# Optimization experiments

Measured on AMD Instinct MI355X. Metric: run time of the kernel, lower is better.

The kernel has to match this reference:

```python
import jax, jax.numpy as jnp
import numpy as np

H = 1024
V = 50257
S = 2048


def setup_inputs() -> dict:
    key = jax.random.key(0)
    ks = jax.random.split(key, 20)
    sd = 1.0 / np.sqrt(H)
    inp = {
        "input": jax.random.randint(ks[0], (1,), 0, V, dtype=jnp.int64) if jax.config.jax_enable_x64 else jax.random.randint(ks[0], (1,), 0, V, dtype=jnp.int32),
        "hidden": jax.random.normal(ks[1], (1, 1, H), dtype=jnp.float32),
        "encoder_hiddens": jax.random.normal(ks[2], (S, H), dtype=jnp.float32),
        "emb": jax.random.normal(ks[3], (V, H), dtype=jnp.float32),
        "Ua_w": jax.random.normal(ks[4], (H, H), dtype=jnp.float32) * sd,
        "Ua_b": jax.random.normal(ks[5], (H,), dtype=jnp.float32) * sd,
        "Wa_w": jax.random.normal(ks[6], (H, H), dtype=jnp.float32) * sd,
        "Wa_b": jax.random.normal(ks[7], (H,), dtype=jnp.float32) * sd,
        "va": jax.random.normal(ks[8], (1, H), dtype=jnp.float32),
        "comb_w": jax.random.normal(ks[9], (H, 2 * H), dtype=jnp.float32) * sd,
        "comb_b": jax.random.normal(ks[10], (H,), dtype=jnp.float32) * sd,
        "gru_w_ih": jax.random.normal(ks[11], (3 * H, H), dtype=jnp.float32) * sd,
        "gru_w_hh": jax.random.normal(ks[12], (3 * H, H), dtype=jnp.float32) * sd,
        "gru_b_ih": jax.random.normal(ks[13], (3 * H,), dtype=jnp.float32) * sd,
        "gru_b_hh": jax.random.normal(ks[14], (3 * H,), dtype=jnp.float32) * sd,
        "out_w": jax.random.normal(ks[15], (V, 2 * H), dtype=jnp.float32) * sd,
        "out_b": jax.random.normal(ks[16], (V,), dtype=jnp.float32) * sd,
    }
    return inp


def reference(input, hidden, encoder_hiddens, emb, Ua_w, Ua_b, Wa_w, Wa_b, va,
              comb_w, comb_b, gru_w_ih, gru_w_hh, gru_b_ih, gru_b_hh, out_w, out_b):
    # embedded: [1,1,H]  (dropout is identity in eval / p handled at train time)
    embedded = emb[input].reshape(1, 1, H)
    enc = encoder_hiddens[:, None, :]  # [S,1,H]
    # Bahdanau scores: tanh(Ua(enc) + Wa(hidden)) -> [S,1,H]
    scores = jnp.tanh(enc @ Ua_w.T + Ua_b + hidden @ Wa_w.T + Wa_b)
    # torch.inner(va [1,H], scores [S,1,H]) -> [1,S,1]; softmax over S
    attn_weights = jax.nn.softmax(jnp.einsum('oh,sbh->osb', va, scores), axis=1)
    # context: sum_s attn[1,S,1] * enc[S,H] -> [1,H]
    context = jnp.sum(attn_weights * encoder_hiddens, axis=1)
    # combine + relu -> GRU input x: [1,H]
    x = jax.nn.relu(jnp.concatenate([embedded[0], context], axis=1) @ comb_w.T + comb_b)
    # single GRU cell step (PyTorch gate layout: r, z, n)
    h0 = hidden[0]  # [1,H]
    gi = x @ gru_w_ih.T + gru_b_ih
    gh = h0 @ gru_w_hh.T + gru_b_hh
    i_r, i_z, i_n = jnp.split(gi, 3, axis=1)
    h_r, h_z, h_n = jnp.split(gh, 3, axis=1)
    r = jax.nn.sigmoid(i_r + h_r)
    z = jax.nn.sigmoid(i_z + h_z)
    n = jnp.tanh(i_n + r * h_n)
    h_new = (1.0 - z) * n + z * h0  # [1,H]
    hidden_out = h_new[None]  # [1,1,H]
    cat_output = jnp.concatenate([context, h_new], axis=1)  # [1,2H]
    log_probs = jax.nn.log_softmax(cat_output @ out_w.T + out_b, axis=1)  # [1,V]
    return (log_probs, hidden_out, attn_weights)
```

## Files before the change

### kernel.cpp

```cpp
#include <hip/hip_runtime.h>
#include <math.h>

#define H 1024
#define V 50257
#define S 2048

typedef unsigned short u16;
typedef __attribute__((ext_vector_type(8))) short short8;
typedef __attribute__((ext_vector_type(4))) float floatx4;

__device__ __forceinline__ float b2f(u16 b) {
    union { unsigned int u; float f; } x; x.u = ((unsigned int)b) << 16; return x.f;
}
__device__ __forceinline__ u16 f2b(float f) {
    union { float f; unsigned int u; } x; x.f = f;
    unsigned int r = x.u + 0x7FFFu + ((x.u >> 16) & 1u);
    return (u16)(r >> 16);
}

__global__ void __launch_bounds__(256) matvec_kernel(
    const float* __restrict__ W,
    const float* __restrict__ xa, const int* __restrict__ xa_idx, int Ka,
    const float* __restrict__ xb, int Kb,
    const float* __restrict__ bias1,
    float* __restrict__ out, int rows, int relu_flag)
{
    int wave = threadIdx.x >> 6;
    int lane = threadIdx.x & 63;
    int r = blockIdx.x * 4 + wave;
    if (r >= rows) return;
    const float* Wr = W + (size_t)r * (Ka + Kb);
    if (xa_idx) xa += (size_t)(*xa_idx) * Ka;
    float dot = 0.f;
    for (int base = 0; base < Ka; base += 256) {
        int k = base + lane * 4;
        float4 w4 = *reinterpret_cast<const float4*>(Wr + k);
        float4 a4 = *reinterpret_cast<const float4*>(xa + k);
        dot += w4.x * a4.x + w4.y * a4.y + w4.z * a4.z + w4.w * a4.w;
    }
    for (int base = 0; base < Kb; base += 256) {
        int k = base + lane * 4;
        float4 w4 = *reinterpret_cast<const float4*>(Wr + Ka + k);
        float4 a4 = *reinterpret_cast<const float4*>(xb + k);
        dot += w4.x * a4.x + w4.y * a4.y + w4.z * a4.z + w4.w * a4.w;
    }
    #pragma unroll
    for (int off = 32; off; off >>= 1) dot += __shfl_down(dot, off);
    if (lane == 0) {
        float v = dot + bias1[r];
        if (relu_flag) v = fmaxf(v, 0.f);
        out[r] = v;
    }
}

__global__ void __launch_bounds__(256) prep_kernel(
    const float* __restrict__ Wa_w, const float* __restrict__ hidden,
    const float* __restrict__ Wa_b, const float* __restrict__ Ua_b,
    float* __restrict__ u_vec, float* __restrict__ ws_zero,
    const float* __restrict__ enc, const float* __restrict__ Ua,
    u16* __restrict__ enc_hi, u16* __restrict__ enc_lo,
    u16* __restrict__ Ua_hi, u16* __restrict__ Ua_lo)
{
    unsigned int zidx = blockIdx.x * 256 + threadIdx.x;
    if (zidx < 4097) ws_zero[zidx] = 0.f;

    if (blockIdx.x < 256) {
        int wave = threadIdx.x >> 6, lane = threadIdx.x & 63;
        int r = blockIdx.x * 4 + wave;
        const float* Wr = Wa_w + (size_t)r * H;
        float dot = 0.f;
        #pragma unroll
        for (int t = 0; t < 4; t++) {
            int k = t * 256 + lane * 4;
            float4 w4 = *reinterpret_cast<const float4*>(Wr + k);
            float4 a4 = *reinterpret_cast<const float4*>(hidden + k);
            dot += w4.x * a4.x + w4.y * a4.y + w4.z * a4.z + w4.w * a4.w;
        }
        #pragma unroll
        for (int off = 32; off; off >>= 1) dot += __shfl_down(dot, off);
        if (lane == 0) u_vec[r] = dot + Wa_b[r] + Ua_b[r];
        return;
    }
    int idx = (blockIdx.x - 256) * 1024 + threadIdx.x * 4;
    const float* src; u16 *dhi, *dlo; int off;
    if (idx < S * H) { src = enc; dhi = enc_hi; dlo = enc_lo; off = idx; }
    else             { src = Ua;  dhi = Ua_hi;  dlo = Ua_lo;  off = idx - S * H; }
    float4 a = *reinterpret_cast<const float4*>(src + off);
    float av[4] = {a.x, a.y, a.z, a.w};
    ushort4 hi4, lo4;
    u16 hv[4], lv[4];
    #pragma unroll
    for (int i = 0; i < 4; i++) {
        u16 h = f2b(av[i]);
        hv[i] = h;
        lv[i] = f2b(av[i] - b2f(h));
    }
    hi4.x = hv[0]; hi4.y = hv[1]; hi4.z = hv[2]; hi4.w = hv[3];
    lo4.x = lv[0]; lo4.y = lv[1]; lo4.z = lv[2]; lo4.w = lv[3];
    *reinterpret_cast<ushort4*>(dhi + off) = hi4;
    *reinterpret_cast<ushort4*>(dlo + off) = lo4;
}

__global__ void __launch_bounds__(256) attn_scores_kernel(
    const u16* __restrict__ enc_hi, const u16* __restrict__ enc_lo,
    const u16* __restrict__ Ua_hi, const u16* __restrict__ Ua_lo,
    const float* __restrict__ va, const float* __restrict__ u,
    float* __restrict__ attn_logits)
{
    int sgrp  = blockIdx.x & 15;
    int jtile = blockIdx.x >> 4;
    int wave = threadIdx.x >> 6;
    int lane = threadIdx.x & 63;
    int l15 = lane & 15, quad = lane >> 4;
    int s0 = sgrp * 128 + wave * 32, j0 = jtile * 64;

    floatx4 zero4 = {0.f, 0.f, 0.f, 0.f};
    floatx4 acc[2][4];
    #pragma unroll
    for (int ra = 0; ra < 2; ra++)
        #pragma unroll
        for (int cb = 0; cb < 4; cb++) acc[ra][cb] = zero4;

    size_t aoff = (size_t)(s0 + l15) * H + quad * 8;
    size_t boff = (size_t)(j0 + l15) * H + quad * 8;

    for (int k0 = 0; k0 < H; k0 += 32) {
        short8 ah0 = *reinterpret_cast<const short8*>(enc_hi + aoff + k0);
        short8 al0 = *reinterpret_cast<const short8*>(enc_lo + aoff + k0);
        short8 ah1 = *reinterpret_cast<const short8*>(enc_hi + aoff + 16 * H + k0);
        short8 al1 = *reinterpret_cast<const short8*>(enc_lo + aoff + 16 * H + k0);
        #pragma unroll
        for (int cb = 0; cb < 4; cb++) {
            size_t bo = boff + (size_t)cb * 16 * H + k0;
            short8 bh = *reinterpret_cast<const short8*>(Ua_hi + bo);
            short8 bl = *reinterpret_cast<const short8*>(Ua_lo + bo);
            acc[0][cb] = __builtin_amdgcn_mfma_f32_16x16x32_bf16(ah0, bh, acc[0][cb], 0, 0, 0);
            acc[0][cb] = __builtin_amdgcn_mfma_f32_16x16x32_bf16(ah0, bl, acc[0][cb], 0, 0, 0);
            acc[0][cb] = __builtin_amdgcn_mfma_f32_16x16x32_bf16(al0, bh, acc[0][cb], 0, 0, 0);
            acc[1][cb] = __builtin_amdgcn_mfma_f32_16x16x32_bf16(ah1, bh, acc[1][cb], 0, 0, 0);
            acc[1][cb] = __builtin_amdgcn_mfma_f32_16x16x32_bf16(ah1, bl, acc[1][cb], 0, 0, 0);
            acc[1][cb] = __builtin_amdgcn_mfma_f32_16x16x32_bf16(al1, bh, acc[1][cb], 0, 0, 0);
        }
    }

    #pragma unroll
    for (int ra = 0; ra < 2; ra++) {
        #pragma unroll
        for (int reg = 0; reg < 4; reg++) {
            float p = 0.f;
            #pragma unroll
            for (int cb = 0; cb < 4; cb++) {
                int jj = j0 + cb * 16 + l15;
                p += va[jj] * tanhf(acc[ra][cb][reg] + u[jj]);
            }
            p += __shfl_xor(p, 1); p += __shfl_xor(p, 2);
            p += __shfl_xor(p, 4); p += __shfl_xor(p, 8);
            if (l15 == 0)
                atomicAdd(&attn_logits[s0 + ra * 16 + quad * 4 + reg], p);
        }
    }
}

__global__ void attn_softmax_kernel(float* __restrict__ logits,
                                    float* __restrict__ attn_out)
{
    __shared__ float red[256];
    int tid = threadIdx.x;
    float vals[8];
    float m = -1e30f;
    #pragma unroll
    for (int i = 0; i < 8; i++) { vals[i] = logits[tid + 256 * i]; m = fmaxf(m, vals[i]); }
    red[tid] = m; __syncthreads();
    for (int s = 128; s > 0; s >>= 1) {
        if (tid < s) red[tid] = fmaxf(red[tid], red[tid + s]);
        __syncthreads();
    }
    float gmax = red[0]; __syncthreads();
    float sum = 0.f;
    #pragma unroll
    for (int i = 0; i < 8; i++) { vals[i] = expf(vals[i] - gmax); sum += vals[i]; }
    red[tid] = sum; __syncthreads();
    for (int s = 128; s > 0; s >>= 1) {
        if (tid < s) red[tid] += red[tid + s];
        __syncthreads();
    }
    float inv = 1.f / red[0];
    #pragma unroll
    for (int i = 0; i < 8; i++) {
        float w = vals[i] * inv;
        logits[tid + 256 * i] = w;
        attn_out[tid + 256 * i] = w;
    }
}

__global__ void __launch_bounds__(256) context_kernel(
    const float* __restrict__ attnw, const float* __restrict__ enc,
    float* __restrict__ ctx)
{
    int h = threadIdx.x * 4;
    int sbase = blockIdx.x * 32;
    float p0 = 0.f, p1 = 0.f, p2 = 0.f, p3 = 0.f;
    for (int i = 0; i < 32; i++) {
        int s = sbase + i;
        float w = attnw[s];
        float4 e = *reinterpret_cast<const float4*>(enc + (size_t)s * H + h);
        p0 = fmaf(w, e.x, p0); p1 = fmaf(w, e.y, p1);
        p2 = fmaf(w, e.z, p2); p3 = fmaf(w, e.w, p3);
    }
    atomicAdd(&ctx[h + 0], p0); atomicAdd(&ctx[h + 1], p1);
    atomicAdd(&ctx[h + 2], p2); atomicAdd(&ctx[h + 3], p3);
}

__global__ void __launch_bounds__(256) gru_fused_kernel(
    const float* __restrict__ w_ih, const float* __restrict__ w_hh,
    const float* __restrict__ x, const float* __restrict__ h0,
    const float* __restrict__ b_ih, const float* __restrict__ b_hh,
    float* __restrict__ cat_hnew, float* __restrict__ out_hidden)
{
    int wave = threadIdx.x >> 6, lane = threadIdx.x & 63;
    int j = blockIdx.x * 4 + wave;
    float d[6] = {0.f, 0.f, 0.f, 0.f, 0.f, 0.f};
    #pragma unroll
    for (int t = 0; t < 4; t++) {
        int k = t * 256 + lane * 4;
        float4 xv = *reinterpret_cast<const float4*>(x + k);
        float4 hv = *reinterpret_cast<const float4*>(h0 + k);
        #pragma unroll
        for (int g = 0; g < 3; g++) {
            float4 wi = *reinterpret_cast<const float4*>(w_ih + (size_t)(g * H + j) * H + k);
            float4 wh = *reinterpret_cast<const float4*>(w_hh + (size_t)(g * H + j) * H + k);
            d[g]     += wi.x * xv.x + wi.y * xv.y + wi.z * xv.z + wi.w * xv.w;
            d[3 + g] += wh.x * hv.x + wh.y * hv.y + wh.z * hv.z + wh.w * hv.w;
        }
    }
    #pragma unroll
    for (int off = 32; off; off >>= 1)
        #pragma unroll
        for (int g = 0; g < 6; g++) d[g] += __shfl_down(d[g], off);
    if (lane == 0) {
        float i_r = d[0] + b_ih[j];
        float i_z = d[1] + b_ih[H + j];
        float i_n = d[2] + b_ih[2 * H + j];
        float h_r = d[3] + b_hh[j];
        float h_z = d[4] + b_hh[H + j];
        float h_n = d[5] + b_hh[2 * H + j];
        float r = 1.f / (1.f + expf(-(i_r + h_r)));
        float z = 1.f / (1.f + expf(-(i_z + h_z)));
        float n = tanhf(i_n + r * h_n);
        float hn = (1.f - z) * n + z * h0[j];
        cat_hnew[j] = hn;
        out_hidden[j] = hn;
    }
}

__global__ void __launch_bounds__(256) out_matvec_kernel(
    const float* __restrict__ Wout, const float* __restrict__ bout,
    const float* __restrict__ cat, float* __restrict__ logits,
    float* __restrict__ sumexp)
{
    __shared__ float cs[2 * H];
    for (int i = threadIdx.x; i < 2 * H; i += 256) cs[i] = cat[i];
    __syncthreads();
    int wave = threadIdx.x >> 6, lane = threadIdx.x & 63;
    float lsum = 0.f;
    for (int v = blockIdx.x * 4 + wave; v < V; v += gridDim.x * 4) {
        const float* Wr = Wout + (size_t)v * (2 * H);
        float dot = 0.f;
        #pragma unroll
        for (int t = 0; t < 8; t++) {
            int k = t * 256 + lane * 4;
            float4 w4 = *reinterpret_cast<const float4*>(Wr + k);
            dot += w4.x * cs[k] + w4.y * cs[k + 1] + w4.z * cs[k + 2] + w4.w * cs[k + 3];
        }
        #pragma unroll
        for (int off = 32; off; off >>= 1) dot += __shfl_down(dot, off);
        if (lane == 0) {
            dot += bout[v];
            logits[v] = dot;
            lsum += expf(dot);
        }
    }
    if (lane == 0) atomicAdd(sumexp, lsum);
}

__global__ void logsoftmax_kernel(float* __restrict__ logits,
                                  const float* __restrict__ sumexp)
{
    int v = blockIdx.x * 256 + threadIdx.x;
    if (v < V) logits[v] -= logf(sumexp[0]);
}

extern "C" void kernel_launch(void* const* d_in, const int* in_sizes, int n_in,
                              void* d_out, int out_size, void* d_ws, size_t ws_size,
                              hipStream_t stream)
{
    const int*   token  = (const int*)d_in[0];
    const float* hidden = (const float*)d_in[1];
    const float* enc    = (const float*)d_in[2];
    const float* emb    = (const float*)d_in[3];
    const float* Ua_w   = (const float*)d_in[4];
    const float* Ua_b   = (const float*)d_in[5];
    const float* Wa_w   = (const float*)d_in[6];
    const float* Wa_b   = (const float*)d_in[7];
    const float* va     = (const float*)d_in[8];
    const float* comb_w = (const float*)d_in[9];
    const float* comb_b = (const float*)d_in[10];
    const float* w_ih   = (const float*)d_in[11];
    const float* w_hh   = (const float*)d_in[12];
    const float* b_ih   = (const float*)d_in[13];
    const float* b_hh   = (const float*)d_in[14];
    const float* out_w  = (const float*)d_in[15];
    const float* out_b  = (const float*)d_in[16];
    float* out = (float*)d_out;

    float* ws          = (float*)d_ws;
    float* attn_logits = ws + 0;
    float* cat         = ws + 2048;
    float* sumexp      = ws + 4096;
    float* u_vec       = ws + 4608;
    float* x_vec       = ws + 5632;

    char* wsb   = (char*)d_ws;
    u16* enc_hi = (u16*)(wsb + 65536);
    u16* enc_lo = (u16*)(wsb + 65536 + 4u * 1024 * 1024);
    u16* Ua_hi  = (u16*)(wsb + 65536 + 8u * 1024 * 1024);
    u16* Ua_lo  = (u16*)(wsb + 65536 + 10u * 1024 * 1024);

    prep_kernel<<<3328, 256, 0, stream>>>(Wa_w, hidden, Wa_b, Ua_b, u_vec, ws,
                                          enc, Ua_w, enc_hi, enc_lo, Ua_hi, Ua_lo);
    attn_scores_kernel<<<256, 256, 0, stream>>>(enc_hi, enc_lo, Ua_hi, Ua_lo,
                                                va, u_vec, attn_logits);
    attn_softmax_kernel<<<1, 256, 0, stream>>>(attn_logits, out + V + H);
    context_kernel<<<64, 256, 0, stream>>>(attn_logits, enc, cat);
    matvec_kernel<<<256, 256, 0, stream>>>(comb_w, emb, token, H, cat, H,
                                           comb_b, x_vec, H, 1);
    gru_fused_kernel<<<256, 256, 0, stream>>>(w_ih, w_hh, x_vec, hidden,
                                              b_ih, b_hh, cat + H, out + V);
    out_matvec_kernel<<<2048, 256, 0, stream>>>(out_w, out_b, cat, out, sumexp);
    logsoftmax_kernel<<<(V + 255) / 256, 256, 0, stream>>>(out, sumexp);
}
```

Measured before the change: 816.8 us.

## Fuse attention softmax into context kernel and replace sumexp atomics with partials

Merges the single-block attention softmax and the context reduction into one 128-block kernel. Each block recomputes the full softmax max and sum redundantly, then scales its own 16 encoder rows, which removes a launch and a serial single-block stage. The output matvec now writes per-block partial exp sums instead of atomically adding to one scalar. Every block of the log-softmax kernel then reduces the 2048 partials itself, adding redundant reads per block but avoiding atomic contention and the need to zero the sum.

Result: faster. 751.2 us (-8.0%).

```diff
diff --git a/kernel.cpp b/kernel.cpp
--- a/kernel.cpp
+++ b/kernel.cpp
@@ -161,10 +161,12 @@
     }
 }
 
-__global__ void attn_softmax_kernel(float* __restrict__ logits,
-                                    float* __restrict__ attn_out)
+__global__ void __launch_bounds__(256) softmax_context_kernel(
+    const float* __restrict__ logits, const float* __restrict__ enc,
+    float* __restrict__ ctx, float* __restrict__ attn_out)
 {
     __shared__ float red[256];
+    __shared__ float sw[16];
     int tid = threadIdx.x;
     float vals[8];
     float m = -1e30f;
@@ -185,25 +187,22 @@
         __syncthreads();
     }
     float inv = 1.f / red[0];
-    #pragma unroll
-    for (int i = 0; i < 8; i++) {
-        float w = vals[i] * inv;
-        logits[tid + 256 * i] = w;
-        attn_out[tid + 256 * i] = w;
-    }
-}
-
-__global__ void __launch_bounds__(256) context_kernel(
-    const float* __restrict__ attnw, const float* __restrict__ enc,
-    float* __restrict__ ctx)
-{
-    int h = threadIdx.x * 4;
-    int sbase = blockIdx.x * 32;
+
+    if (blockIdx.x == 0) {
+        #pragma unroll
+        for (int i = 0; i < 8; i++) attn_out[tid + 256 * i] = vals[i] * inv;
+    }
+
+    int sbase = blockIdx.x * 16;
+    if (tid < 16) sw[tid] = expf(logits[sbase + tid] - gmax) * inv;
+    __syncthreads();
+
+    int h = tid * 4;
     float p0 = 0.f, p1 = 0.f, p2 = 0.f, p3 = 0.f;
-    for (int i = 0; i < 32; i++) {
-        int s = sbase + i;
-        float w = attnw[s];
-        float4 e = *reinterpret_cast<const float4*>(enc + (size_t)s * H + h);
+    #pragma unroll
+    for (int i = 0; i < 16; i++) {
+        float w = sw[i];
+        float4 e = *reinterpret_cast<const float4*>(enc + (size_t)(sbase + i) * H + h);
         p0 = fmaf(w, e.x, p0); p1 = fmaf(w, e.y, p1);
         p2 = fmaf(w, e.z, p2); p3 = fmaf(w, e.w, p3);
     }
@@ -256,9 +255,10 @@
 __global__ void __launch_bounds__(256) out_matvec_kernel(
     const float* __restrict__ Wout, const float* __restrict__ bout,
     const float* __restrict__ cat, float* __restrict__ logits,
-    float* __restrict__ sumexp)
+    float* __restrict__ separtial)
 {
     __shared__ float cs[2 * H];
+    __shared__ float wred[4];
     for (int i = threadIdx.x; i < 2 * H; i += 256) cs[i] = cat[i];
     __syncthreads();
     int wave = threadIdx.x >> 6, lane = threadIdx.x & 63;
@@ -280,14 +280,28 @@
             lsum += expf(dot);
         }
     }
-    if (lane == 0) atomicAdd(sumexp, lsum);
-}
-
-__global__ void logsoftmax_kernel(float* __restrict__ logits,
-                                  const float* __restrict__ sumexp)
-{
-    int v = blockIdx.x * 256 + threadIdx.x;
-    if (v < V) logits[v] -= logf(sumexp[0]);
+    if (lane == 0) wred[wave] = lsum;
+    __syncthreads();
+    if (threadIdx.x == 0)
+        separtial[blockIdx.x] = wred[0] + wred[1] + wred[2] + wred[3];
+}
+
+__global__ void __launch_bounds__(256) logsoftmax_kernel(
+    float* __restrict__ logits, const float* __restrict__ separtial)
+{
+    __shared__ float red[256];
+    int tid = threadIdx.x;
+    float s = 0.f;
+    #pragma unroll
+    for (int i = 0; i < 8; i++) s += separtial[tid + 256 * i];
+    red[tid] = s; __syncthreads();
+    for (int st = 128; st > 0; st >>= 1) {
+        if (tid < st) red[tid] += red[tid + st];
+        __syncthreads();
+    }
+    float lz = logf(red[0]);
+    int v = blockIdx.x * 256 + tid;
+    if (v < V) logits[v] -= lz;
 }
 
 extern "C" void kernel_launch(void* const* d_in, const int* in_sizes, int n_in,
@@ -316,9 +330,9 @@
     float* ws          = (float*)d_ws;
     float* attn_logits = ws + 0;
     float* cat         = ws + 2048;
-    float* sumexp      = ws + 4096;
     float* u_vec       = ws + 4608;
     float* x_vec       = ws + 5632;
+    float* separtial   = ws + 6656;
 
     char* wsb   = (char*)d_ws;
     u16* enc_hi = (u16*)(wsb + 65536);
@@ -330,12 +344,12 @@
                                           enc, Ua_w, enc_hi, enc_lo, Ua_hi, Ua_lo);
     attn_scores_kernel<<<256, 256, 0, stream>>>(enc_hi, enc_lo, Ua_hi, Ua_lo,
                                                 va, u_vec, attn_logits);
-    attn_softmax_kernel<<<1, 256, 0, stream>>>(attn_logits, out + V + H);
-    context_kernel<<<64, 256, 0, stream>>>(attn_logits, enc, cat);
+    softmax_context_kernel<<<128, 256, 0, stream>>>(attn_logits, enc, cat,
+                                                    out + V + H);
     matvec_kernel<<<256, 256, 0, stream>>>(comb_w, emb, token, H, cat, H,
                                            comb_b, x_vec, H, 1);
     gru_fused_kernel<<<256, 256, 0, stream>>>(w_ih, w_hh, x_vec, hidden,
                                               b_ih, b_hh, cat + H, out + V);
-    out_matvec_kernel<<<2048, 256, 0, stream>>>(out_w, out_b, cat, out, sumexp);
-    logsoftmax_kernel<<<(V + 255) / 256, 256, 0, stream>>>(out, sumexp);
-}
+    out_matvec_kernel<<<2048, 256, 0, stream>>>(out_w, out_b, cat, out, separtial);
+    logsoftmax_kernel<<<(V + 255) / 256, 256, 0, stream>>>(out, separtial);
+}
```
